# Kernel optimization log

Measured on AMD Instinct MI355X. Metric: run time of the kernel, lower is better.

## Reference

```python
import jax, jax.numpy as jnp
import numpy as np

NEG_INF = -9.0e15  # matches torch's -9000000000000000.0 mask value
ALPHA = 0.2        # LeakyReLU negative slope


def setup_inputs() -> dict:
    key = jax.random.key(0)
    k1, k2, k3, k4 = jax.random.split(key, 4)
    N, F_in, F_out = 8192, 128, 128
    x = jax.random.normal(k1, (N, F_in), dtype=jnp.float32)
    adj = jax.random.randint(k2, (N, N), 0, 2, dtype=jnp.int32)
    W = jax.random.normal(k3, (F_in, F_out), dtype=jnp.float32) * (1.0 / np.sqrt(F_in))
    a = jax.random.normal(k4, (2 * F_out, 1), dtype=jnp.float32) * (1.0 / np.sqrt(2 * F_out))
    return {"x": x, "adj": adj, "W": W, "a": a}


def reference(x, adj, W, a):
    # h = W(input): [N, F_out]
    h = x @ W
    F_out = h.shape[1]
    # a([h_i || h_j]) = h_i . a[:F] + h_j . a[F:]  -- identical math to the
    # original NxNx2F concat, without materializing it.
    a_src = a[:F_out, 0]   # coefficients on the row (i) node
    a_dst = a[F_out:, 0]   # coefficients on the column (j) node
    s_src = h @ a_src      # [N]
    s_dst = h @ a_dst      # [N]
    e = jax.nn.leaky_relu(s_src[:, None] + s_dst[None, :], negative_slope=ALPHA)  # [N, N]
    e = jnp.where(adj > 0, e, jnp.float32(NEG_INF))
    attention = jax.nn.softmax(e, axis=1)
    # dropout omitted (identity at eval) for a deterministic baseline
    h_prime = attention @ h  # [N, F_out]
    return h_prime
```

## Files before the change

kernel.cpp:

```cpp
#include <hip/hip_runtime.h>

#define N 8192
#define F 128
#define NS 4
#define JT (N / NS)
#define CJ 64
#define NC (JT / CJ)
#define TI 32
#define WT_STRIDE 72
#define ALPHA 0.2f

typedef __attribute__((ext_vector_type(8))) short short8;
typedef __attribute__((ext_vector_type(4))) float f32x4;
typedef unsigned short u16;

__device__ __forceinline__ u16 f2bf(float f) {
    unsigned int u = __float_as_uint(f);
    u += 0x7fff + ((u >> 16) & 1);
    return (u16)(u >> 16);
}
__device__ __forceinline__ float bf2f(u16 b) {
    return __uint_as_float(((unsigned int)b) << 16);
}
__device__ __forceinline__ float lrelu(float z) { return fmaxf(z, ALPHA * z); }

__device__ __forceinline__ void dma16(const void* g, void* l) {
    __builtin_amdgcn_global_load_lds((__attribute__((address_space(1))) void*)g,
                                     (__attribute__((address_space(3))) void*)l, 16, 0, 0);
}

__global__ __launch_bounds__(256) void gemm_h(const float* __restrict__ x,
                                              const float* __restrict__ W,
                                              const float* __restrict__ aa,
                                              u16* __restrict__ hT,
                                              float* __restrict__ ssrc,
                                              float* __restrict__ sdst) {
    __shared__ float xs[32 * 128];
    __shared__ float Wsh[32 * 128];
    const int t = threadIdx.x;
    const int i0 = blockIdx.x * 32;
    const int c4 = (t & 31) * 4;
    const int r8 = t >> 5;

#pragma unroll
    for (int p = 0; p < 4; ++p) {
        int rr = p * 8 + r8;
        *(float4*)&xs[rr * 128 + c4] = *(const float4*)&x[(size_t)(i0 + rr) * 128 + c4];
    }

    const int tx = t & 31, ty = t >> 5;
    const int r0 = ty * 4, c0 = tx * 4;
    float acc[4][4] = {};

    for (int kc = 0; kc < 4; ++kc) {
        __syncthreads();
#pragma unroll
        for (int p = 0; p < 4; ++p) {
            int k = p * 8 + r8;
            *(float4*)&Wsh[k * 128 + c4] = *(const float4*)&W[(kc * 32 + k) * 128 + c4];
        }
        __syncthreads();
#pragma unroll 4
        for (int k = 0; k < 32; k += 4) {
            float xr[4][4];
#pragma unroll
            for (int rr = 0; rr < 4; ++rr)
                *(float4*)xr[rr] = *(const float4*)&xs[(r0 + rr) * 128 + kc * 32 + k];
#pragma unroll
            for (int kk = 0; kk < 4; ++kk) {
                float4 wv = *(const float4*)&Wsh[(k + kk) * 128 + c0];
#pragma unroll
                for (int rr = 0; rr < 4; ++rr) {
                    acc[rr][0] += xr[rr][kk] * wv.x;
                    acc[rr][1] += xr[rr][kk] * wv.y;
                    acc[rr][2] += xr[rr][kk] * wv.z;
                    acc[rr][3] += xr[rr][kk] * wv.w;
                }
            }
        }
    }

#pragma unroll
    for (int rr = 0; rr < 4; ++rr)
#pragma unroll
        for (int cc = 0; cc < 4; ++cc)
            hT[(size_t)(c0 + cc) * N + (i0 + r0 + rr)] = f2bf(acc[rr][cc]);

    float4 asv = *(const float4*)&aa[c0];
    float4 adv = *(const float4*)&aa[F + c0];
#pragma unroll
    for (int rr = 0; rr < 4; ++rr) {
        float vs = acc[rr][0] * asv.x + acc[rr][1] * asv.y + acc[rr][2] * asv.z + acc[rr][3] * asv.w;
        float vd = acc[rr][0] * adv.x + acc[rr][1] * adv.y + acc[rr][2] * adv.z + acc[rr][3] * adv.w;
#pragma unroll
        for (int off = 16; off >= 1; off >>= 1) {
            vs += __shfl_down(vs, off, 32);
            vd += __shfl_down(vd, off, 32);
        }
        if (tx == 0) {
            ssrc[i0 + r0 + rr] = vs;
            sdst[i0 + r0 + rr] = vd;
        }
    }
}

__global__ __launch_bounds__(256, 4) void attn_mfma(const int* __restrict__ adj,
                                                    const u16* __restrict__ hT,
                                                    const float* __restrict__ ssrc,
                                                    const float* __restrict__ sdst,
                                                    float* __restrict__ pacc,
                                                    float* __restrict__ pS) {
    __shared__ u16 bt[2][128 * CJ];
    __shared__ u16 wt[TI * WT_STRIDE];

    const int t = threadIdx.x;
    const int w = t >> 6, L = t & 63;
    const int quad = L >> 4, l16 = L & 15;
    const int i0 = blockIdx.x * TI;
    const int split = blockIdx.y;
    const int j0 = split * JT;

    const int ar = t >> 4;
    const int ac = (t & 15) * 4;
    const float s_i0 = ssrc[i0 + ar];
    const float s_i1 = ssrc[i0 + 16 + ar];
    const size_t arow0 = (size_t)(i0 + ar) * N;
    const size_t arow1 = (size_t)(i0 + 16 + ar) * N;

    const int bf = t >> 3;
    const int bsj = (t & 7) ^ (bf & 7);
    const size_t bgoff = (size_t)bf * N + j0 + bsj * 8;

    const int rt = w & 1;
    const int colbase = (w >> 1) * 4;

    f32x4 acc[4];
#pragma unroll
    for (int ci = 0; ci < 4; ++ci) acc[ci] = 0.f;
    float sum0 = 0.f, sum1 = 0.f;

#pragma unroll
    for (int rp = 0; rp < 4; ++rp)
        dma16(hT + bgoff + (size_t)rp * 32 * N, &bt[0][rp * 2048 + w * 512]);
    int4 a0 = *(const int4*)(adj + arow0 + j0 + ac);
    int4 a1 = *(const int4*)(adj + arow1 + j0 + ac);
    float4 dv = *(const float4*)(sdst + j0 + ac);

    for (int c = 0; c < NC; ++c) {
        ushort4 wlo, whi;
        {
            int m0[4] = {a0.x, a0.y, a0.z, a0.w};
            int m1[4] = {a1.x, a1.y, a1.z, a1.w};
            float d[4] = {dv.x, dv.y, dv.z, dv.w};
            u16 q0[4], q1[4];
#pragma unroll
            for (int k = 0; k < 4; ++k) {
                float e0 = __expf(lrelu(s_i0 + d[k]));
                float e1 = __expf(lrelu(s_i1 + d[k]));
                q0[k] = f2bf(m0[k] > 0 ? e0 : 0.f);
                q1[k] = f2bf(m1[k] > 0 ? e1 : 0.f);
                sum0 += bf2f(q0[k]);
                sum1 += bf2f(q1[k]);
            }
            wlo = {q0[0], q0[1], q0[2], q0[3]};
            whi = {q1[0], q1[1], q1[2], q1[3]};
        }

        __syncthreads();
        *(ushort4*)&wt[ar * WT_STRIDE + ac] = wlo;
        *(ushort4*)&wt[(16 + ar) * WT_STRIDE + ac] = whi;
        __syncthreads();

        const int cn = (c + 1 < NC) ? c + 1 : c;
        const size_t jn = (size_t)cn * CJ;
        {
            u16* dstb = bt[(c + 1) & 1];
#pragma unroll
            for (int rp = 0; rp < 4; ++rp)
                dma16(hT + bgoff + (size_t)rp * 32 * N + jn, &dstb[rp * 2048 + w * 512]);
        }
        a0 = *(const int4*)(adj + arow0 + j0 + jn + ac);
        a1 = *(const int4*)(adj + arow1 + j0 + jn + ac);
        dv = *(const float4*)(sdst + j0 + jn + ac);

        const u16* btc = bt[c & 1];
#pragma unroll
        for (int ks = 0; ks < 2; ++ks) {
            short8 A = *(const short8*)&wt[(rt * 16 + l16) * WT_STRIDE + ks * 32 + quad * 8];
#pragma unroll
            for (int ci = 0; ci < 4; ++ci) {
                const int f = (colbase + ci) * 16 + l16;
                const int s = (ks * 4 + quad) ^ (f & 7);
                short8 B = *(const short8*)&btc[(f >> 5) * 2048 + (f & 31) * 64 + s * 8];
                acc[ci] = __builtin_amdgcn_mfma_f32_16x16x32_bf16(A, B, acc[ci], 0, 0, 0);
            }
        }
    }

    float* dst = pacc + (size_t)split * N * F;
#pragma unroll
    for (int ci = 0; ci < 4; ++ci) {
        const int col = (colbase + ci) * 16 + l16;
        const int r0 = i0 + rt * 16 + quad * 4;
#pragma unroll
        for (int r = 0; r < 4; ++r)
            dst[(size_t)(r0 + r) * F + col] = acc[ci][r];
    }

#pragma unroll
    for (int off = 8; off >= 1; off >>= 1) {
        sum0 += __shfl_down(sum0, off, 16);
        sum1 += __shfl_down(sum1, off, 16);
    }
    if ((t & 15) == 0) {
        pS[(size_t)split * N + i0 + ar] = sum0;
        pS[(size_t)split * N + i0 + 16 + ar] = sum1;
    }
}

__global__ __launch_bounds__(256) void finalize(float* __restrict__ out,
                                                const float* __restrict__ pacc,
                                                const float* __restrict__ pS) {
    const int idx = (blockIdx.x * 256 + threadIdx.x) * 4;
    const int i = idx >> 7;
    float s = 0.f;
#pragma unroll
    for (int k = 0; k < NS; ++k) s += pS[(size_t)k * N + i];
    float4 a = {0.f, 0.f, 0.f, 0.f};
#pragma unroll
    for (int k = 0; k < NS; ++k) {
        float4 v = *(const float4*)&pacc[(size_t)k * N * F + idx];
        a.x += v.x; a.y += v.y; a.z += v.z; a.w += v.w;
    }
    const float inv = 1.0f / s;
    float4 o = {a.x * inv, a.y * inv, a.z * inv, a.w * inv};
    *(float4*)&out[idx] = o;
}

extern "C" void kernel_launch(void* const* d_in, const int* in_sizes, int n_in,
                              void* d_out, int out_size, void* d_ws, size_t ws_size,
                              hipStream_t stream) {
    (void)in_sizes; (void)n_in; (void)out_size; (void)ws_size;
    const float* x   = (const float*)d_in[0];
    const int*   adj = (const int*)d_in[1];
    const float* W   = (const float*)d_in[2];
    const float* a   = (const float*)d_in[3];
    float* out = (float*)d_out;

    u16* hT     = (u16*)d_ws;
    float* ssrc = (float*)(hT + (size_t)N * F);
    float* sdst = ssrc + N;
    float* pS   = sdst + N;
    float* pacc = pS + (size_t)NS * N;

    gemm_h<<<N / 32, 256, 0, stream>>>(x, W, a, hT, ssrc, sdst);
    attn_mfma<<<dim3(N / TI, NS), 256, 0, stream>>>(adj, hT, ssrc, sdst, pacc, pS);
    finalize<<<(N * F / 4) / 256, 256, 0, stream>>>(out, pacc, pS);
}
```

Baseline: 414.8 us.

## Build MFMA A operand from attention weights in registers, dropping LDS staging

```diff
diff --git a/kernel.cpp b/kernel.cpp
--- a/kernel.cpp
+++ b/kernel.cpp
@@ -7,7 +7,6 @@
 #define CJ 64
 #define NC (JT / CJ)
 #define TI 32
-#define WT_STRIDE 72
 #define ALPHA 0.2f
 
 typedef __attribute__((ext_vector_type(8))) short short8;
@@ -111,7 +110,6 @@
                                                     float* __restrict__ pacc,
                                                     float* __restrict__ pS) {
     __shared__ u16 bt[2][128 * CJ];
-    __shared__ u16 wt[TI * WT_STRIDE];
 
     const int t = threadIdx.x;
     const int w = t >> 6, L = t & 63;
@@ -120,81 +118,86 @@
     const int split = blockIdx.y;
     const int j0 = split * JT;
 
-    const int ar = t >> 4;
-    const int ac = (t & 15) * 4;
-    const float s_i0 = ssrc[i0 + ar];
-    const float s_i1 = ssrc[i0 + 16 + ar];
-    const size_t arow0 = (size_t)(i0 + ar) * N;
-    const size_t arow1 = (size_t)(i0 + 16 + ar) * N;
+    const int rt = w & 1;
+    const int colbase = (w >> 1) * 4;
+    const int row = i0 + rt * 16 + l16;
+    const float s_i = ssrc[row];
+
+    const int* pA = adj + (size_t)row * N + j0 + quad * 8;
+    const float* pD = sdst + j0 + quad * 8;
 
     const int bf = t >> 3;
     const int bsj = (t & 7) ^ (bf & 7);
-    const size_t bgoff = (size_t)bf * N + j0 + bsj * 8;
-
-    const int rt = w & 1;
-    const int colbase = (w >> 1) * 4;
+    const u16* pG = hT + (size_t)bf * N + j0 + bsj * 8;
 
     f32x4 acc[4];
 #pragma unroll
     for (int ci = 0; ci < 4; ++ci) acc[ci] = 0.f;
-    float sum0 = 0.f, sum1 = 0.f;
+    float rsum = 0.f;
+
+    int4 aj[2][2][2];
+    float4 dd[2][2][2];
 
 #pragma unroll
     for (int rp = 0; rp < 4; ++rp)
-        dma16(hT + bgoff + (size_t)rp * 32 * N, &bt[0][rp * 2048 + w * 512]);
-    int4 a0 = *(const int4*)(adj + arow0 + j0 + ac);
-    int4 a1 = *(const int4*)(adj + arow1 + j0 + ac);
-    float4 dv = *(const float4*)(sdst + j0 + ac);
+        dma16(pG + (size_t)rp * 32 * N, &bt[0][rp * 2048 + w * 512]);
+#pragma unroll
+    for (int ks = 0; ks < 2; ++ks) {
+        aj[0][ks][0] = *(const int4*)(pA + ks * 32);
+        aj[0][ks][1] = *(const int4*)(pA + ks * 32 + 4);
+        dd[0][ks][0] = *(const float4*)(pD + ks * 32);
+        dd[0][ks][1] = *(const float4*)(pD + ks * 32 + 4);
+    }
+    __syncthreads();
 
     for (int c = 0; c < NC; ++c) {
-        ushort4 wlo, whi;
+        const int cn = (c + 1 < NC) ? c + 1 : c;
+        const int sl = (c + 1) & 1;
+
         {
-            int m0[4] = {a0.x, a0.y, a0.z, a0.w};
-            int m1[4] = {a1.x, a1.y, a1.z, a1.w};
-            float d[4] = {dv.x, dv.y, dv.z, dv.w};
-            u16 q0[4], q1[4];
-#pragma unroll
-            for (int k = 0; k < 4; ++k) {
-                float e0 = __expf(lrelu(s_i0 + d[k]));
-                float e1 = __expf(lrelu(s_i1 + d[k]));
-                q0[k] = f2bf(m0[k] > 0 ? e0 : 0.f);
-                q1[k] = f2bf(m1[k] > 0 ? e1 : 0.f);
-                sum0 += bf2f(q0[k]);
-                sum1 += bf2f(q1[k]);
+            u16* db = bt[sl];
+#pragma unroll
+            for (int rp = 0; rp < 4; ++rp)
+                dma16(pG + (size_t)rp * 32 * N + cn * CJ, &db[rp * 2048 + w * 512]);
+        }
+#pragma unroll
+        for (int ks = 0; ks < 2; ++ks) {
+            aj[sl][ks][0] = *(const int4*)(pA + cn * CJ + ks * 32);
+            aj[sl][ks][1] = *(const int4*)(pA + cn * CJ + ks * 32 + 4);
+            dd[sl][ks][0] = *(const float4*)(pD + cn * CJ + ks * 32);
+            dd[sl][ks][1] = *(const float4*)(pD + cn * CJ + ks * 32 + 4);
+        }
+
+        short8 A[2];
+#pragma unroll
+        for (int ks = 0; ks < 2; ++ks) {
+            const int s = c & 1;
+            int m[8] = {aj[s][ks][0].x, aj[s][ks][0].y, aj[s][ks][0].z, aj[s][ks][0].w,
+                        aj[s][ks][1].x, aj[s][ks][1].y, aj[s][ks][1].z, aj[s][ks][1].w};
+            float d[8] = {dd[s][ks][0].x, dd[s][ks][0].y, dd[s][ks][0].z, dd[s][ks][0].w,
+                          dd[s][ks][1].x, dd[s][ks][1].y, dd[s][ks][1].z, dd[s][ks][1].w};
+#pragma unroll
+            for (int k = 0; k < 8; ++k) {
+                float e = __expf(lrelu(s_i + d[k]));
+                u16 b = f2bf(m[k] > 0 ? e : 0.f);
+                rsum += bf2f(b);
+                A[ks][k] = (short)b;
             }
-            wlo = {q0[0], q0[1], q0[2], q0[3]};
-            whi = {q1[0], q1[1], q1[2], q1[3]};
-        }
-
-        __syncthreads();
-        *(ushort4*)&wt[ar * WT_STRIDE + ac] = wlo;
-        *(ushort4*)&wt[(16 + ar) * WT_STRIDE + ac] = whi;
-        __syncthreads();
-
-        const int cn = (c + 1 < NC) ? c + 1 : c;
-        const size_t jn = (size_t)cn * CJ;
-        {
-            u16* dstb = bt[(c + 1) & 1];
-#pragma unroll
-            for (int rp = 0; rp < 4; ++rp)
-                dma16(hT + bgoff + (size_t)rp * 32 * N + jn, &dstb[rp * 2048 + w * 512]);
-        }
-        a0 = *(const int4*)(adj + arow0 + j0 + jn + ac);
-        a1 = *(const int4*)(adj + arow1 + j0 + jn + ac);
-        dv = *(const float4*)(sdst + j0 + jn + ac);
+        }
 
         const u16* btc = bt[c & 1];
 #pragma unroll
         for (int ks = 0; ks < 2; ++ks) {
-            short8 A = *(const short8*)&wt[(rt * 16 + l16) * WT_STRIDE + ks * 32 + quad * 8];
 #pragma unroll
             for (int ci = 0; ci < 4; ++ci) {
                 const int f = (colbase + ci) * 16 + l16;
                 const int s = (ks * 4 + quad) ^ (f & 7);
                 short8 B = *(const short8*)&btc[(f >> 5) * 2048 + (f & 31) * 64 + s * 8];
-                acc[ci] = __builtin_amdgcn_mfma_f32_16x16x32_bf16(A, B, acc[ci], 0, 0, 0);
+                acc[ci] = __builtin_amdgcn_mfma_f32_16x16x32_bf16(A[ks], B, acc[ci], 0, 0, 0);
             }
         }
+
+        __syncthreads();
     }
 
     float* dst = pacc + (size_t)split * N * F;
@@ -207,15 +210,10 @@
             dst[(size_t)(r0 + r) * F + col] = acc[ci][r];
     }
 
-#pragma unroll
-    for (int off = 8; off >= 1; off >>= 1) {
-        sum0 += __shfl_down(sum0, off, 16);
-        sum1 += __shfl_down(sum1, off, 16);
-    }
-    if ((t & 15) == 0) {
-        pS[(size_t)split * N + i0 + ar] = sum0;
-        pS[(size_t)split * N + i0 + 16 + ar] = sum1;
-    }
+    rsum += __shfl_xor(rsum, 16);
+    rsum += __shfl_xor(rsum, 32);
+    if (w < 2 && L < 16)
+        pS[(size_t)split * N + i0 + rt * 16 + l16] = rsum;
 }
 
 __global__ __launch_bounds__(256) void finalize(float* __restrict__ out,
```

Result: slower. 844.8 us (+103.7%).
